# Performance work log

Hardware: AMD Instinct MI355X
Metric: run time of the kernel (lower is better)

## Reference

```python
import jax, jax.numpy as jnp
import numpy as np

B, S, D, H = 32, 2048, 128, 16  # batch, cached kv len, head dim (=d_model), heads
EPS = 1e-5


def setup_inputs() -> dict:
    key = jax.random.key(0)
    ks = jax.random.split(key, 5)
    d_total = D * H
    x = jax.random.normal(ks[0], (B, 1, D), jnp.float32)
    past_k = jax.random.normal(ks[1], (B, H, S, D), jnp.float32)
    past_v = jax.random.normal(ks[2], (B, H, S, D), jnp.float32)
    Wqkv = jax.random.normal(ks[3], (3 * d_total, D), jnp.float32) * 0.02
    bqkv = jnp.zeros((3 * d_total,), jnp.float32)
    Wout = jax.random.normal(ks[4], (D, d_total), jnp.float32) * 0.02
    bout = jnp.zeros((D,), jnp.float32)
    return {"x": x, "past_k": past_k, "past_v": past_v,
            "Wqkv": Wqkv, "bqkv": bqkv, "Wout": Wout, "bout": bout}


def reference(x, past_k, past_v, Wqkv, bqkv, Wout, bout):
    # QKV projection: (B,1,D) -> (B,1,3*H*D)
    qkv = x @ Wqkv.T + bqkv
    qkv = qkv.reshape(B, 1, 3 * H, D).transpose(0, 2, 1, 3)  # (B,3H,1,D)
    q, k_new, v_new = jnp.split(qkv, 3, axis=1)              # each (B,H,1,D)
    k = jnp.concatenate([past_k, k_new], axis=2)             # (B,H,S+1,D)
    v = jnp.concatenate([past_v, v_new], axis=2)
    # single-query attention (causal mask is trivially all-visible for q_len=1)
    scale = 1.0 / jnp.sqrt(jnp.float32(D))
    scores = jnp.einsum('bhqd,bhkd->bhqk', q, k) * scale     # (B,H,1,S+1)
    probs = jax.nn.softmax(scores, axis=-1)
    y = jnp.einsum('bhqk,bhkd->bhqd', probs, v)              # (B,H,1,D)
    y = y.transpose(0, 2, 1, 3).reshape(B, 1, H * D)         # (B,1,H*D)
    y = y @ Wout.T + bout                                    # (B,1,D)
    y = y + x                                                # residual
    # layer norm over last dim, no affine params
    mu = jnp.mean(y, axis=-1, keepdims=True)
    var = jnp.mean(jnp.square(y - mu), axis=-1, keepdims=True)
    out = (y - mu) / jnp.sqrt(var + EPS)
    return (out, k, v)
```

## Files before the change

### kernel.cpp

```cpp
#include <hip/hip_runtime.h>
#include <math.h>

#define B 32
#define S 2048
#define S1 2049
#define D 128
#define H 16
#define DT 2048
#define NS 4
#define RPS 512
#define EPS 1e-5f
#define SCALE 0.08838834764831845f

typedef float f4v __attribute__((ext_vector_type(4)));

__global__ void __launch_bounds__(256)
qkv_proj_kernel(const float* __restrict__ x,
                const float* __restrict__ Wqkv,
                const float* __restrict__ bqkv,
                float* __restrict__ qkv,
                float* __restrict__ out_k,
                float* __restrict__ out_v) {
    const int b = blockIdx.x;
    const int j = blockIdx.y * 256 + threadIdx.x;
    __shared__ float xs[D];
    if (threadIdx.x < D) xs[threadIdx.x] = x[b * D + threadIdx.x];
    __syncthreads();
    const float* w = Wqkv + (size_t)j * D;
    float acc = bqkv[j];
#pragma unroll
    for (int d = 0; d < D; d += 4) {
        float4 w4 = *reinterpret_cast<const float4*>(w + d);
        acc = fmaf(w4.x, xs[d + 0], acc);
        acc = fmaf(w4.y, xs[d + 1], acc);
        acc = fmaf(w4.z, xs[d + 2], acc);
        acc = fmaf(w4.w, xs[d + 3], acc);
    }
    qkv[(size_t)b * (3 * DT) + j] = acc;

    if (j >= DT) {
        const int r = j - DT;
        const int which = r >> 11;
        const int hd = r & (DT - 1);
        const int h = hd >> 7;
        const int d = hd & 127;
        float* dst = which ? out_v : out_k;
        dst[((size_t)(b * H + h) * S1 + S) * D + d] = acc;
    }
}

__global__ void __launch_bounds__(256)
attn_kernel(const float* __restrict__ past_k,
            const float* __restrict__ past_v,
            const float* __restrict__ qkv,
            float* __restrict__ out_k,
            float* __restrict__ out_v,
            float* __restrict__ part_ml,
            float* __restrict__ part_acc) {
    const int bx = blockIdx.x;
    const int split = bx & (NS - 1);
    const int bh = bx >> 2;
    const int b = bh >> 4;
    const int h = bh & (H - 1);
    const int tid  = threadIdx.x;
    const int wave = tid >> 6;
    const int lane = tid & 63;
    const int half = lane >> 5;
    const int l32  = lane & 31;
    const int rg   = wave * 2 + half;

    __shared__ float sc[RPS];
    __shared__ float swm[4];
    __shared__ float swl[4];
    __shared__ float sacc[8 * D];

    const f4v* __restrict__ kin  = (const f4v*)past_k + (size_t)(b * H + h) * S * 32;
    const f4v* __restrict__ vin  = (const f4v*)past_v + (size_t)(b * H + h) * S * 32;
    f4v* __restrict__ kout = (f4v*)out_k + (size_t)(b * H + h) * S1 * 32;
    f4v* __restrict__ vout = (f4v*)out_v + (size_t)(b * H + h) * S1 * 32;

    const f4v q4 = ((const f4v*)qkv)[(size_t)b * (3 * DT / 4) + h * 32 + l32];

    const size_t base = (size_t)split * RPS * 32;

#pragma unroll 8
    for (int it = 0; it < RPS / 8; ++it) {
        const int r = it * 8 + rg;
        const size_t off = base + (size_t)r * 32 + l32;
        f4v k4 = __builtin_nontemporal_load(&kin[off]);
        __builtin_nontemporal_store(k4, &kout[off]);
        f4v t = k4 * q4;
        float p = t.x + t.y + t.z + t.w;
        p += __shfl_xor(p, 1);
        p += __shfl_xor(p, 2);
        p += __shfl_xor(p, 4);
        p += __shfl_xor(p, 8);
        p += __shfl_xor(p, 16);
        if (l32 == 0) sc[r] = p * SCALE;
    }
    __syncthreads();

    float s0v = sc[tid];
    float s1v = sc[tid + 256];
    float m = fmaxf(s0v, s1v);
#pragma unroll
    for (int off = 1; off < 64; off <<= 1) m = fmaxf(m, __shfl_xor(m, off));
    if (lane == 0) swm[wave] = m;
    __syncthreads();
    const float M = fmaxf(fmaxf(swm[0], swm[1]), fmaxf(swm[2], swm[3]));
    const float e0 = __expf(s0v - M);
    const float e1 = __expf(s1v - M);
    sc[tid] = e0;
    sc[tid + 256] = e1;
    float lsum = e0 + e1;
#pragma unroll
    for (int off = 1; off < 64; off <<= 1) lsum += __shfl_xor(lsum, off);
    if (lane == 0) swl[wave] = lsum;
    __syncthreads();
    const float L = swl[0] + swl[1] + swl[2] + swl[3];

    f4v acc = (f4v){0.f, 0.f, 0.f, 0.f};
#pragma unroll 8
    for (int it = 0; it < RPS / 8; ++it) {
        const int r = it * 8 + rg;
        const size_t off = base + (size_t)r * 32 + l32;
        f4v v4 = __builtin_nontemporal_load(&vin[off]);
        __builtin_nontemporal_store(v4, &vout[off]);
        const float p = sc[r];
        acc += v4 * p;
    }

    ((f4v*)sacc)[rg * 32 + l32] = acc;
    __syncthreads();

    if (tid < D) {
        float y = 0.f;
#pragma unroll
        for (int g = 0; g < 8; ++g) y += sacc[g * D + tid];
        part_acc[(size_t)bx * D + tid] = y;
        if (tid == 0) {
            part_ml[2 * bx + 0] = M;
            part_ml[2 * bx + 1] = L;
        }
    }
}

__global__ void __launch_bounds__(1024)
out_proj_kernel(const float* __restrict__ x,
                const float* __restrict__ qkv,
                const float* __restrict__ part_ml,
                const float* __restrict__ part_acc,
                const float* __restrict__ Wout,
                const float* __restrict__ bout,
                float* __restrict__ out) {
    const int b = blockIdx.x;
    const int t = threadIdx.x;
    __shared__ float ys[DT];
    __shared__ float pp[D * 8];
    __shared__ float tb[D];

    {
        const int h = t >> 6;
        const int lane = t & 63;
        const float* qp   = qkv + (size_t)b * (3 * DT) + h * D;
        const float* knew = qp + DT;
        const float* vnew = qp + 2 * DT;
        float pd = qp[2 * lane] * knew[2 * lane] + qp[2 * lane + 1] * knew[2 * lane + 1];
        pd += __shfl_xor(pd, 1);
        pd += __shfl_xor(pd, 2);
        pd += __shfl_xor(pd, 4);
        pd += __shfl_xor(pd, 8);
        pd += __shfl_xor(pd, 16);
        pd += __shfl_xor(pd, 32);
        const float s = pd * SCALE;

        const int bh = b * H + h;
        float m0 = part_ml[2 * (bh * NS + 0)], l0 = part_ml[2 * (bh * NS + 0) + 1];
        float m1 = part_ml[2 * (bh * NS + 1)], l1 = part_ml[2 * (bh * NS + 1) + 1];
        float m2 = part_ml[2 * (bh * NS + 2)], l2 = part_ml[2 * (bh * NS + 2) + 1];
        float m3 = part_ml[2 * (bh * NS + 3)], l3 = part_ml[2 * (bh * NS + 3) + 1];
        float M = fmaxf(fmaxf(fmaxf(m0, m1), fmaxf(m2, m3)), s);
        const float w0 = __expf(m0 - M), w1 = __expf(m1 - M);
        const float w2 = __expf(m2 - M), w3 = __expf(m3 - M);
        const float wn = __expf(s - M);
        const float L = w0 * l0 + w1 * l1 + w2 * l2 + w3 * l3 + wn;
        const float invL = 1.0f / L;
#pragma unroll
        for (int r = 0; r < 2; ++r) {
            const int d = lane + r * 64;
            float y = wn * vnew[d];
            y = fmaf(w0, part_acc[(size_t)(bh * NS + 0) * D + d], y);
            y = fmaf(w1, part_acc[(size_t)(bh * NS + 1) * D + d], y);
            y = fmaf(w2, part_acc[(size_t)(bh * NS + 2) * D + d], y);
            y = fmaf(w3, part_acc[(size_t)(bh * NS + 3) * D + d], y);
            ys[h * D + d] = y * invL;
        }
    }
    __syncthreads();

    {
        const int d = t >> 3;
        const int sub = t & 7;
        const float* w = Wout + (size_t)d * DT + sub * 256;
        const float* y = ys + sub * 256;
        float acc = 0.f;
#pragma unroll
        for (int j = 0; j < 256; j += 4) {
            float4 w4 = *reinterpret_cast<const float4*>(w + j);
            acc = fmaf(w4.x, y[j + 0], acc);
            acc = fmaf(w4.y, y[j + 1], acc);
            acc = fmaf(w4.z, y[j + 2], acc);
            acc = fmaf(w4.w, y[j + 3], acc);
        }
        pp[d * 8 + sub] = acc;
    }
    __syncthreads();

    float val = 0.f;
    if (t < D) {
        float a = 0.f;
#pragma unroll
        for (int g = 0; g < 8; ++g) a += pp[t * 8 + g];
        val = a + bout[t] + x[b * D + t];
        tb[t] = val;
    }
    __syncthreads();
    for (int off = 64; off > 0; off >>= 1) {
        if (t < off) tb[t] += tb[t + off];
        __syncthreads();
    }
    const float mu = tb[0] * (1.0f / D);
    __syncthreads();
    const float diff = val - mu;
    if (t < D) tb[t] = diff * diff;
    __syncthreads();
    for (int off = 64; off > 0; off >>= 1) {
        if (t < off) tb[t] += tb[t + off];
        __syncthreads();
    }
    const float var = tb[0] * (1.0f / D);
    if (t < D) out[(size_t)b * D + t] = diff / sqrtf(var + EPS);
}

extern "C" void kernel_launch(void* const* d_in, const int* in_sizes, int n_in,
                              void* d_out, int out_size, void* d_ws, size_t ws_size,
                              hipStream_t stream) {
    const float* x      = (const float*)d_in[0];
    const float* past_k = (const float*)d_in[1];
    const float* past_v = (const float*)d_in[2];
    const float* Wqkv   = (const float*)d_in[3];
    const float* bqkv   = (const float*)d_in[4];
    const float* Wout   = (const float*)d_in[5];
    const float* bout   = (const float*)d_in[6];

    float* out   = (float*)d_out;
    float* out_k = out + (size_t)B * D;
    float* out_v = out_k + (size_t)B * H * S1 * D;

    float* qkv      = (float*)d_ws;
    float* part_ml  = qkv + (size_t)B * 3 * DT;
    float* part_acc = part_ml + 2 * B * H * NS;

    qkv_proj_kernel<<<dim3(B, (3 * DT) / 256), 256, 0, stream>>>(
        x, Wqkv, bqkv, qkv, out_k, out_v);
    attn_kernel<<<B * H * NS, 256, 0, stream>>>(
        past_k, past_v, qkv, out_k, out_v, part_ml, part_acc);
    out_proj_kernel<<<B, 1024, 0, stream>>>(
        x, qkv, part_ml, part_acc, Wout, bout, out);
}
```

Baseline: 468.8 us.

## Drop split-KV in attention; use one 1024-thread block per head and finalize softmax in-kernel

The attention kernel no longer splits each (batch, head) across four 256-thread blocks. It runs one 1024-thread block per head over the full 2048-row cache and folds the new-token score and value in directly. The merge of partial max/sum and accumulators moves out of the output-projection kernel, which now just loads the normalized head outputs from workspace. This removes the partial-result round trip and merge math, but grid size drops from 2048 to 512 blocks, and each block now needs more LDS and a longer serial loop. Those could reduce memory-level parallelism in this bandwidth-bound copy-plus-attention pass.

Result: faster. 445.3 us (-5.0%).

```diff
diff --git a/kernel.cpp b/kernel.cpp
--- a/kernel.cpp
+++ b/kernel.cpp
@@ -7,8 +7,6 @@
 #define D 128
 #define H 16
 #define DT 2048
-#define NS 4
-#define RPS 512
 #define EPS 1e-5f
 #define SCALE 0.08838834764831845f
 
@@ -49,44 +47,42 @@
     }
 }
 
-__global__ void __launch_bounds__(256)
+__global__ void __launch_bounds__(1024)
 attn_kernel(const float* __restrict__ past_k,
             const float* __restrict__ past_v,
             const float* __restrict__ qkv,
             float* __restrict__ out_k,
             float* __restrict__ out_v,
-            float* __restrict__ part_ml,
-            float* __restrict__ part_acc) {
-    const int bx = blockIdx.x;
-    const int split = bx & (NS - 1);
-    const int bh = bx >> 2;
+            float* __restrict__ ys_g) {
+    const int bh = blockIdx.x;
     const int b = bh >> 4;
     const int h = bh & (H - 1);
     const int tid  = threadIdx.x;
     const int wave = tid >> 6;
     const int lane = tid & 63;
-    const int half = lane >> 5;
-    const int l32  = lane & 31;
-    const int rg   = wave * 2 + half;
-
-    __shared__ float sc[RPS];
-    __shared__ float swm[4];
-    __shared__ float swl[4];
-    __shared__ float sacc[8 * D];
-
-    const f4v* __restrict__ kin  = (const f4v*)past_k + (size_t)(b * H + h) * S * 32;
-    const f4v* __restrict__ vin  = (const f4v*)past_v + (size_t)(b * H + h) * S * 32;
-    f4v* __restrict__ kout = (f4v*)out_k + (size_t)(b * H + h) * S1 * 32;
-    f4v* __restrict__ vout = (f4v*)out_v + (size_t)(b * H + h) * S1 * 32;
-
-    const f4v q4 = ((const f4v*)qkv)[(size_t)b * (3 * DT / 4) + h * 32 + l32];
-
-    const size_t base = (size_t)split * RPS * 32;
+    const int l32  = tid & 31;
+    const int rg   = tid >> 5;
+
+    __shared__ float sc[S1 + 3];
+    __shared__ float swm[16];
+    __shared__ float swl[16];
+    __shared__ float sacc[32 * D];
+
+    const f4v* __restrict__ kin  = (const f4v*)past_k + (size_t)bh * S * 32;
+    const f4v* __restrict__ vin  = (const f4v*)past_v + (size_t)bh * S * 32;
+    f4v* __restrict__ kout = (f4v*)out_k + (size_t)bh * S1 * 32;
+    f4v* __restrict__ vout = (f4v*)out_v + (size_t)bh * S1 * 32;
+
+    const float* qp   = qkv + (size_t)b * (3 * DT) + h * D;
+    const float* knew = qp + DT;
+    const float* vnew = qp + 2 * DT;
+
+    const f4v q4 = ((const f4v*)qp)[l32];
 
 #pragma unroll 8
-    for (int it = 0; it < RPS / 8; ++it) {
-        const int r = it * 8 + rg;
-        const size_t off = base + (size_t)r * 32 + l32;
+    for (int it = 0; it < S / 32; ++it) {
+        const int r = it * 32 + rg;
+        const size_t off = (size_t)r * 32 + l32;
         f4v k4 = __builtin_nontemporal_load(&kin[off]);
         __builtin_nontemporal_store(k4, &kout[off]);
         f4v t = k4 * q4;
@@ -98,36 +94,56 @@
         p += __shfl_xor(p, 16);
         if (l32 == 0) sc[r] = p * SCALE;
     }
-    __syncthreads();
-
-    float s0v = sc[tid];
-    float s1v = sc[tid + 256];
-    float m = fmaxf(s0v, s1v);
+    if (tid < 64) {
+        float pd = qp[2 * tid] * knew[2 * tid] + qp[2 * tid + 1] * knew[2 * tid + 1];
+        pd += __shfl_xor(pd, 1);
+        pd += __shfl_xor(pd, 2);
+        pd += __shfl_xor(pd, 4);
+        pd += __shfl_xor(pd, 8);
+        pd += __shfl_xor(pd, 16);
+        pd += __shfl_xor(pd, 32);
+        if (tid == 0) sc[S] = pd * SCALE;
+    }
+    __syncthreads();
+
+    const float s0v = sc[tid];
+    const float s1v = sc[tid + 1024];
+    const float sxv = (tid == 0) ? sc[S] : -1e30f;
+    float m = fmaxf(fmaxf(s0v, s1v), sxv);
 #pragma unroll
     for (int off = 1; off < 64; off <<= 1) m = fmaxf(m, __shfl_xor(m, off));
     if (lane == 0) swm[wave] = m;
     __syncthreads();
-    const float M = fmaxf(fmaxf(swm[0], swm[1]), fmaxf(swm[2], swm[3]));
+    float M = swm[0];
+#pragma unroll
+    for (int g = 1; g < 16; ++g) M = fmaxf(M, swm[g]);
     const float e0 = __expf(s0v - M);
     const float e1 = __expf(s1v - M);
     sc[tid] = e0;
-    sc[tid + 256] = e1;
+    sc[tid + 1024] = e1;
     float lsum = e0 + e1;
+    if (tid == 0) {
+        const float e2 = __expf(sxv - M);
+        sc[S] = e2;
+        lsum += e2;
+    }
 #pragma unroll
     for (int off = 1; off < 64; off <<= 1) lsum += __shfl_xor(lsum, off);
     if (lane == 0) swl[wave] = lsum;
     __syncthreads();
-    const float L = swl[0] + swl[1] + swl[2] + swl[3];
+    float L = swl[0];
+#pragma unroll
+    for (int g = 1; g < 16; ++g) L += swl[g];
+    const float invL = 1.0f / L;
 
     f4v acc = (f4v){0.f, 0.f, 0.f, 0.f};
 #pragma unroll 8
-    for (int it = 0; it < RPS / 8; ++it) {
-        const int r = it * 8 + rg;
-        const size_t off = base + (size_t)r * 32 + l32;
+    for (int it = 0; it < S / 32; ++it) {
+        const int r = it * 32 + rg;
+        const size_t off = (size_t)r * 32 + l32;
         f4v v4 = __builtin_nontemporal_load(&vin[off]);
         __builtin_nontemporal_store(v4, &vout[off]);
-        const float p = sc[r];
-        acc += v4 * p;
+        acc += v4 * sc[r];
     }
 
     ((f4v*)sacc)[rg * 32 + l32] = acc;
@@ -136,20 +152,15 @@
     if (tid < D) {
         float y = 0.f;
 #pragma unroll
-        for (int g = 0; g < 8; ++g) y += sacc[g * D + tid];
-        part_acc[(size_t)bx * D + tid] = y;
-        if (tid == 0) {
-            part_ml[2 * bx + 0] = M;
-            part_ml[2 * bx + 1] = L;
-        }
+        for (int g = 0; g < 32; ++g) y += sacc[g * D + tid];
+        y = fmaf(sc[S], vnew[tid], y);
+        ys_g[(size_t)bh * D + tid] = y * invL;
     }
 }
 
 __global__ void __launch_bounds__(1024)
 out_proj_kernel(const float* __restrict__ x,
-                const float* __restrict__ qkv,
-                const float* __restrict__ part_ml,
-                const float* __restrict__ part_acc,
+                const float* __restrict__ ys_g,
                 const float* __restrict__ Wout,
                 const float* __restrict__ bout,
                 float* __restrict__ out) {
@@ -159,43 +170,8 @@
     __shared__ float pp[D * 8];
     __shared__ float tb[D];
 
-    {
-        const int h = t >> 6;
-        const int lane = t & 63;
-        const float* qp   = qkv + (size_t)b * (3 * DT) + h * D;
-        const float* knew = qp + DT;
-        const float* vnew = qp + 2 * DT;
-        float pd = qp[2 * lane] * knew[2 * lane] + qp[2 * lane + 1] * knew[2 * lane + 1];
-        pd += __shfl_xor(pd, 1);
-        pd += __shfl_xor(pd, 2);
-        pd += __shfl_xor(pd, 4);
-        pd += __shfl_xor(pd, 8);
-        pd += __shfl_xor(pd, 16);
-        pd += __shfl_xor(pd, 32);
-        const float s = pd * SCALE;
-
-        const int bh = b * H + h;
-        float m0 = part_ml[2 * (bh * NS + 0)], l0 = part_ml[2 * (bh * NS + 0) + 1];
-        float m1 = part_ml[2 * (bh * NS + 1)], l1 = part_ml[2 * (bh * NS + 1) + 1];
-        float m2 = part_ml[2 * (bh * NS + 2)], l2 = part_ml[2 * (bh * NS + 2) + 1];
-        float m3 = part_ml[2 * (bh * NS + 3)], l3 = part_ml[2 * (bh * NS + 3) + 1];
-        float M = fmaxf(fmaxf(fmaxf(m0, m1), fmaxf(m2, m3)), s);
-        const float w0 = __expf(m0 - M), w1 = __expf(m1 - M);
-        const float w2 = __expf(m2 - M), w3 = __expf(m3 - M);
-        const float wn = __expf(s - M);
-        const float L = w0 * l0 + w1 * l1 + w2 * l2 + w3 * l3 + wn;
-        const float invL = 1.0f / L;
-#pragma unroll
-        for (int r = 0; r < 2; ++r) {
-            const int d = lane + r * 64;
-            float y = wn * vnew[d];
-            y = fmaf(w0, part_acc[(size_t)(bh * NS + 0) * D + d], y);
-            y = fmaf(w1, part_acc[(size_t)(bh * NS + 1) * D + d], y);
-            y = fmaf(w2, part_acc[(size_t)(bh * NS + 2) * D + d], y);
-            y = fmaf(w3, part_acc[(size_t)(bh * NS + 3) * D + d], y);
-            ys[h * D + d] = y * invL;
-        }
-    }
+    ys[t]        = ys_g[(size_t)b * DT + t];
+    ys[t + 1024] = ys_g[(size_t)b * DT + t + 1024];
     __syncthreads();
 
     {
@@ -257,14 +233,13 @@
     float* out_k = out + (size_t)B * D;
     float* out_v = out_k + (size_t)B * H * S1 * D;
 
-    float* qkv      = (float*)d_ws;
-    float* part_ml  = qkv + (size_t)B * 3 * DT;
-    float* part_acc = part_ml + 2 * B * H * NS;
+    float* qkv  = (float*)d_ws;
+    float* ys_g = qkv + (size_t)B * 3 * DT;
 
     qkv_proj_kernel<<<dim3(B, (3 * DT) / 256), 256, 0, stream>>>(
         x, Wqkv, bqkv, qkv, out_k, out_v);
-    attn_kernel<<<B * H * NS, 256, 0, stream>>>(
-        past_k, past_v, qkv, out_k, out_v, part_ml, part_acc);
+    attn_kernel<<<B * H, 1024, 0, stream>>>(
+        past_k, past_v, qkv, out_k, out_v, ys_g);
     out_proj_kernel<<<B, 1024, 0, stream>>>(
-        x, qkv, part_ml, part_acc, Wout, bout, out);
-}
+        x, ys_g, Wout, bout, out);
+}
```
